# Kernel optimization log

Measured on AMD Instinct MI355X. Metric: run time of the kernel, lower is better.

## Reference

```python
import jax, jax.numpy as jnp
import numpy as np

TOP_K = 2

def setup_inputs() -> dict:
    key = jax.random.key(0)
    k1, k2 = jax.random.split(key)
    x = jax.random.normal(k1, (4, 4096, 4096), dtype=jnp.float32)
    # nn.Linear(hidden, experts, bias=False) weight: [num_experts, hidden]
    gate_w = jax.random.normal(k2, (64, 4096), dtype=jnp.float32) * (1.0 / np.sqrt(4096.0))
    return {"x": x, "gate_w": gate_w}

def reference(x, gate_w):
    # logits: [b, s, e] = x @ gate_w.T
    logits = jnp.einsum('bsh,eh->bse', x, gate_w)
    top_k_logits, top_k_indices = jax.lax.top_k(logits, TOP_K)  # [b, s, k]
    # softmax over top-k logits in float32, cast back to logits dtype
    probs = jax.nn.softmax(top_k_logits.astype(jnp.float32), axis=-1).astype(logits.dtype)
    return (logits, top_k_indices, probs)
```

## Files before the change

### kernel.cpp

```cpp
#include <hip/hip_runtime.h>
#include <math.h>

#define H 4096
#define E 64
#define BMROWS 32
#define NT 256
#define KQ 1024
#define BK 32
#define NWIN (KQ / BK)

typedef short bf16x8 __attribute__((ext_vector_type(8)));
typedef float f32x4  __attribute__((ext_vector_type(4)));

__device__ __forceinline__ unsigned f2bf_rne_u(float f) {
    unsigned u = __float_as_uint(f);
    return (u + 0x7fffu + ((u >> 16) & 1u)) >> 16;
}

__global__ __launch_bounds__(256) void convert_w(const float* __restrict__ w,
                                                 unsigned short* __restrict__ wh,
                                                 unsigned short* __restrict__ wl) {
    const int i = (blockIdx.x * 256 + threadIdx.x) * 4;
    float4 v = *(const float4*)(w + i);
    float vv[4] = {v.x, v.y, v.z, v.w};
    unsigned hh[4], ll[4];
#pragma unroll
    for (int j = 0; j < 4; ++j) {
        hh[j] = f2bf_rne_u(vv[j]);
        float r = vv[j] - __uint_as_float(hh[j] << 16);
        ll[j] = __float_as_uint(r) >> 16;
    }
    ushort4 h, l;
    h.x = (unsigned short)hh[0]; h.y = (unsigned short)hh[1];
    h.z = (unsigned short)hh[2]; h.w = (unsigned short)hh[3];
    l.x = (unsigned short)ll[0]; l.y = (unsigned short)ll[1];
    l.z = (unsigned short)ll[2]; l.w = (unsigned short)ll[3];
    *(ushort4*)(wh + i) = h;
    *(ushort4*)(wl + i) = l;
}

__device__ __forceinline__ void cvt8(const float4 a, const float4 b,
                                     bf16x8& hi, bf16x8& lo) {
    float v[8] = {a.x, a.y, a.z, a.w, b.x, b.y, b.z, b.w};
#pragma unroll
    for (int i = 0; i < 8; ++i) {
        unsigned h = f2bf_rne_u(v[i]);
        float r = v[i] - __uint_as_float(h << 16);
        unsigned l = __float_as_uint(r) >> 16;
        hi[i] = (short)h;
        lo[i] = (short)l;
    }
}

__global__ __launch_bounds__(NT, 2) void router_kernel(
    const float* __restrict__ x,
    const unsigned short* __restrict__ wh,
    const unsigned short* __restrict__ wl,
    float* __restrict__ out, int M)
{
    __shared__ __align__(16) f32x4 merge[8][4][64];

    const int t    = threadIdx.x;
    const int lane = t & 63;
    const int wk   = t >> 6;
    const int m0   = blockIdx.x * BMROWS;
    const int col  = lane & 15;
    const int quad = lane >> 4;

    const int kbase = wk * KQ + quad * 8;

    const float* xp0 = x + (size_t)(m0 + col) * H + kbase;
    const float* xp1 = x + (size_t)(m0 + 16 + col) * H + kbase;
    const unsigned short* whp = wh + (size_t)col * H + kbase;
    const unsigned short* wlp = wl + (size_t)col * H + kbase;

    f32x4 acc[2][4];
#pragma unroll
    for (int mt = 0; mt < 2; ++mt)
#pragma unroll
        for (int nt = 0; nt < 4; ++nt)
            acc[mt][nt] = (f32x4){0.0f, 0.0f, 0.0f, 0.0f};

    float4 xr[2][2];
    uint4  wrh[4], wrl[4];

    auto loadwin = [&](int win) {
        const int k = win * BK;
        xr[0][0] = *(const float4*)(xp0 + k);
        xr[0][1] = *(const float4*)(xp0 + k + 4);
        xr[1][0] = *(const float4*)(xp1 + k);
        xr[1][1] = *(const float4*)(xp1 + k + 4);
#pragma unroll
        for (int nt = 0; nt < 4; ++nt) {
            wrh[nt] = *(const uint4*)(whp + (size_t)(nt * 16) * H + k);
            wrl[nt] = *(const uint4*)(wlp + (size_t)(nt * 16) * H + k);
        }
    };

    loadwin(0);
#pragma unroll 2
    for (int win = 0; win < NWIN; ++win) {
        bf16x8 ah[2], al[2];
        cvt8(xr[0][0], xr[0][1], ah[0], al[0]);
        cvt8(xr[1][0], xr[1][1], ah[1], al[1]);
        bf16x8 bh[4], bl[4];
#pragma unroll
        for (int nt = 0; nt < 4; ++nt) {
            bh[nt] = __builtin_bit_cast(bf16x8, wrh[nt]);
            bl[nt] = __builtin_bit_cast(bf16x8, wrl[nt]);
        }

        if (win + 1 < NWIN) loadwin(win + 1);

#pragma unroll
        for (int nt = 0; nt < 4; ++nt) {
#pragma unroll
            for (int mt = 0; mt < 2; ++mt) {
                acc[mt][nt] = __builtin_amdgcn_mfma_f32_16x16x32_bf16(
                    ah[mt], bh[nt], acc[mt][nt], 0, 0, 0);
                acc[mt][nt] = __builtin_amdgcn_mfma_f32_16x16x32_bf16(
                    ah[mt], bl[nt], acc[mt][nt], 0, 0, 0);
                acc[mt][nt] = __builtin_amdgcn_mfma_f32_16x16x32_bf16(
                    al[mt], bh[nt], acc[mt][nt], 0, 0, 0);
            }
        }
    }

#pragma unroll
    for (int mt = 0; mt < 2; ++mt)
#pragma unroll
        for (int nt = 0; nt < 4; ++nt)
            merge[mt * 4 + nt][wk][lane] = acc[mt][nt];
    __syncthreads();

    if (wk != 0) return;

#pragma unroll
    for (int mt = 0; mt < 2; ++mt)
#pragma unroll
        for (int nt = 0; nt < 4; ++nt) {
#pragma unroll
            for (int w = 1; w < 4; ++w) {
                f32x4 o = merge[mt * 4 + nt][w][lane];
                acc[mt][nt] += o;
            }
        }

    float* logits   = out;
    float* idx_out  = out + (size_t)M * E;
    float* prob_out = idx_out + (size_t)M * 2;

#pragma unroll
    for (int mt = 0; mt < 2; ++mt) {
        const int mrow = m0 + mt * 16 + quad * 4;
#pragma unroll
        for (int r = 0; r < 4; ++r) {
#pragma unroll
            for (int nt = 0; nt < 4; ++nt)
                logits[(size_t)(mrow + r) * E + nt * 16 + col] = acc[mt][nt][r];

            float v1 = acc[mt][0][r], v2 = -INFINITY;
            int   i1 = col,           i2 = 0x7fffffff;
#pragma unroll
            for (int nt = 1; nt < 4; ++nt) {
                const float v = acc[mt][nt][r];
                const int   e = nt * 16 + col;
                if (v > v1)      { v2 = v1; i2 = i1; v1 = v; i1 = e; }
                else if (v > v2) { v2 = v;  i2 = e; }
            }
#pragma unroll
            for (int mask = 1; mask < 16; mask <<= 1) {
                const float ov1 = __shfl_xor(v1, mask);
                const float ov2 = __shfl_xor(v2, mask);
                const int   oi1 = __shfl_xor(i1, mask);
                const int   oi2 = __shfl_xor(i2, mask);
                const bool afirst = (v1 > ov1) || (v1 == ov1 && i1 < oi1);
                float nv1, nv2; int ni1, ni2;
                if (afirst) {
                    nv1 = v1; ni1 = i1;
                    const bool s = (v2 > ov1) || (v2 == ov1 && i2 < oi1);
                    nv2 = s ? v2 : ov1; ni2 = s ? i2 : oi1;
                } else {
                    nv1 = ov1; ni1 = oi1;
                    const bool s = (ov2 > v1) || (ov2 == v1 && oi2 < i1);
                    nv2 = s ? ov2 : v1; ni2 = s ? oi2 : i1;
                }
                v1 = nv1; v2 = nv2; i1 = ni1; i2 = ni2;
            }
            if (col == 0) {
                const int m = mrow + r;
                const float e2 = __expf(v2 - v1);
                const float d  = 1.0f + e2;
                *(float2*)(idx_out  + (size_t)m * 2) = make_float2((float)i1, (float)i2);
                *(float2*)(prob_out + (size_t)m * 2) = make_float2(1.0f / d, e2 / d);
            }
        }
    }
}

extern "C" void kernel_launch(void* const* d_in, const int* in_sizes, int n_in,
                              void* d_out, int out_size, void* d_ws, size_t ws_size,
                              hipStream_t stream) {
    const float* x = (const float*)d_in[0];
    const float* w = (const float*)d_in[1];
    unsigned short* wh = (unsigned short*)d_ws;
    unsigned short* wl = wh + (size_t)E * H;
    const int M = in_sizes[0] / H;

    hipLaunchKernelGGL(convert_w, dim3((E * H) / 1024), dim3(256), 0, stream,
                       w, wh, wl);
    hipLaunchKernelGGL(router_kernel, dim3(M / BMROWS), dim3(NT), 0, stream,
                       x, wh, wl, (float*)d_out, M);
}
```

Baseline: 407.3 us.

## Deepen x prefetch to three windows and split epilogue across two waves

The main loop now keeps x loads three windows ahead in four rotating register buffers and double-buffers the weight loads, manually unrolled by four. The goal is to hide more HBM latency on the streamed x input, which dominates traffic. The cross-wave reduction and top-2/softmax epilogue is now split so waves 0 and 1 each handle one 16-row tile instead of wave 0 doing both. The bf16 split conversion is also slightly simplified. The extra register buffers raise VGPR pressure, which may hurt occupancy under launch_bounds(256,2).

Result: no change. 403.4 us (-1.0%).

```diff
diff --git a/kernel.cpp b/kernel.cpp
--- a/kernel.cpp
+++ b/kernel.cpp
@@ -44,11 +44,11 @@
     float v[8] = {a.x, a.y, a.z, a.w, b.x, b.y, b.z, b.w};
 #pragma unroll
     for (int i = 0; i < 8; ++i) {
-        unsigned h = f2bf_rne_u(v[i]);
-        float r = v[i] - __uint_as_float(h << 16);
-        unsigned l = __float_as_uint(r) >> 16;
-        hi[i] = (short)h;
-        lo[i] = (short)l;
+        const unsigned u = __float_as_uint(v[i]);
+        const unsigned t = u + 0x7fffu + ((u >> 16) & 1u);
+        const float    r = v[i] - __uint_as_float(t & 0xffff0000u);
+        hi[i] = (short)(t >> 16);
+        lo[i] = (short)(__float_as_uint(r) >> 16);
     }
 }
 
@@ -81,49 +81,60 @@
         for (int nt = 0; nt < 4; ++nt)
             acc[mt][nt] = (f32x4){0.0f, 0.0f, 0.0f, 0.0f};
 
-    float4 xr[2][2];
-    uint4  wrh[4], wrl[4];
-
-    auto loadwin = [&](int win) {
+    float4 x0[2][2], x1[2][2], x2[2][2], x3[2][2];
+    uint4  wAh[4], wAl[4], wBh[4], wBl[4];
+
+    auto loadx_into = [&](int win, float4 (&xb)[2][2]) {
         const int k = win * BK;
-        xr[0][0] = *(const float4*)(xp0 + k);
-        xr[0][1] = *(const float4*)(xp0 + k + 4);
-        xr[1][0] = *(const float4*)(xp1 + k);
-        xr[1][1] = *(const float4*)(xp1 + k + 4);
+        xb[0][0] = *(const float4*)(xp0 + k);
+        xb[0][1] = *(const float4*)(xp0 + k + 4);
+        xb[1][0] = *(const float4*)(xp1 + k);
+        xb[1][1] = *(const float4*)(xp1 + k + 4);
+    };
+    auto loadw_into = [&](int win, uint4 (&wh_)[4], uint4 (&wl_)[4]) {
+        const int k = win * BK;
 #pragma unroll
         for (int nt = 0; nt < 4; ++nt) {
-            wrh[nt] = *(const uint4*)(whp + (size_t)(nt * 16) * H + k);
-            wrl[nt] = *(const uint4*)(wlp + (size_t)(nt * 16) * H + k);
+            wh_[nt] = *(const uint4*)(whp + (size_t)(nt * 16) * H + k);
+            wl_[nt] = *(const uint4*)(wlp + (size_t)(nt * 16) * H + k);
         }
     };
 
-    loadwin(0);
-#pragma unroll 2
-    for (int win = 0; win < NWIN; ++win) {
+    auto step = [&](int win, float4 (&xc)[2][2], float4 (&xpref)[2][2],
+                    uint4 (&whc)[4], uint4 (&wlc)[4],
+                    uint4 (&whn)[4], uint4 (&wln)[4]) {
+        if (win + 3 < NWIN) loadx_into(win + 3, xpref);
+        if (win + 1 < NWIN) loadw_into(win + 1, whn, wln);
         bf16x8 ah[2], al[2];
-        cvt8(xr[0][0], xr[0][1], ah[0], al[0]);
-        cvt8(xr[1][0], xr[1][1], ah[1], al[1]);
-        bf16x8 bh[4], bl[4];
+        cvt8(xc[0][0], xc[0][1], ah[0], al[0]);
+        cvt8(xc[1][0], xc[1][1], ah[1], al[1]);
 #pragma unroll
         for (int nt = 0; nt < 4; ++nt) {
-            bh[nt] = __builtin_bit_cast(bf16x8, wrh[nt]);
-            bl[nt] = __builtin_bit_cast(bf16x8, wrl[nt]);
-        }
-
-        if (win + 1 < NWIN) loadwin(win + 1);
-
-#pragma unroll
-        for (int nt = 0; nt < 4; ++nt) {
+            const bf16x8 bh = __builtin_bit_cast(bf16x8, whc[nt]);
+            const bf16x8 bl = __builtin_bit_cast(bf16x8, wlc[nt]);
 #pragma unroll
             for (int mt = 0; mt < 2; ++mt) {
                 acc[mt][nt] = __builtin_amdgcn_mfma_f32_16x16x32_bf16(
-                    ah[mt], bh[nt], acc[mt][nt], 0, 0, 0);
+                    ah[mt], bh, acc[mt][nt], 0, 0, 0);
                 acc[mt][nt] = __builtin_amdgcn_mfma_f32_16x16x32_bf16(
-                    ah[mt], bl[nt], acc[mt][nt], 0, 0, 0);
+                    ah[mt], bl, acc[mt][nt], 0, 0, 0);
                 acc[mt][nt] = __builtin_amdgcn_mfma_f32_16x16x32_bf16(
-                    al[mt], bh[nt], acc[mt][nt], 0, 0, 0);
+                    al[mt], bh, acc[mt][nt], 0, 0, 0);
             }
         }
+    };
+
+    loadx_into(0, x0);
+    loadx_into(1, x1);
+    loadx_into(2, x2);
+    loadw_into(0, wAh, wAl);
+
+#pragma unroll 1
+    for (int win = 0; win < NWIN; win += 4) {
+        step(win,     x0, x3, wAh, wAl, wBh, wBl);
+        step(win + 1, x1, x0, wBh, wBl, wAh, wAl);
+        step(win + 2, x2, x1, wAh, wAl, wBh, wBl);
+        step(win + 3, x3, x2, wBh, wBl, wAh, wAl);
     }
 
 #pragma unroll
@@ -133,67 +144,64 @@
             merge[mt * 4 + nt][wk][lane] = acc[mt][nt];
     __syncthreads();
 
-    if (wk != 0) return;
-
-#pragma unroll
-    for (int mt = 0; mt < 2; ++mt)
-#pragma unroll
-        for (int nt = 0; nt < 4; ++nt) {
-#pragma unroll
-            for (int w = 1; w < 4; ++w) {
-                f32x4 o = merge[mt * 4 + nt][w][lane];
-                acc[mt][nt] += o;
-            }
-        }
+    if (wk >= 2) return;
+    const int mt = wk;
+
+    f32x4 a2[4];
+#pragma unroll
+    for (int nt = 0; nt < 4; ++nt) {
+        f32x4 s = merge[mt * 4 + nt][0][lane];
+#pragma unroll
+        for (int w = 1; w < 4; ++w)
+            s += merge[mt * 4 + nt][w][lane];
+        a2[nt] = s;
+    }
 
     float* logits   = out;
     float* idx_out  = out + (size_t)M * E;
     float* prob_out = idx_out + (size_t)M * 2;
 
-#pragma unroll
-    for (int mt = 0; mt < 2; ++mt) {
-        const int mrow = m0 + mt * 16 + quad * 4;
-#pragma unroll
-        for (int r = 0; r < 4; ++r) {
-#pragma unroll
-            for (int nt = 0; nt < 4; ++nt)
-                logits[(size_t)(mrow + r) * E + nt * 16 + col] = acc[mt][nt][r];
-
-            float v1 = acc[mt][0][r], v2 = -INFINITY;
-            int   i1 = col,           i2 = 0x7fffffff;
-#pragma unroll
-            for (int nt = 1; nt < 4; ++nt) {
-                const float v = acc[mt][nt][r];
-                const int   e = nt * 16 + col;
-                if (v > v1)      { v2 = v1; i2 = i1; v1 = v; i1 = e; }
-                else if (v > v2) { v2 = v;  i2 = e; }
+    const int mrow = m0 + mt * 16 + quad * 4;
+#pragma unroll
+    for (int r = 0; r < 4; ++r) {
+#pragma unroll
+        for (int nt = 0; nt < 4; ++nt)
+            logits[(size_t)(mrow + r) * E + nt * 16 + col] = a2[nt][r];
+
+        float v1 = a2[0][r], v2 = -INFINITY;
+        int   i1 = col,      i2 = 0x7fffffff;
+#pragma unroll
+        for (int nt = 1; nt < 4; ++nt) {
+            const float v = a2[nt][r];
+            const int   e = nt * 16 + col;
+            if (v > v1)      { v2 = v1; i2 = i1; v1 = v; i1 = e; }
+            else if (v > v2) { v2 = v;  i2 = e; }
+        }
+#pragma unroll
+        for (int mask = 1; mask < 16; mask <<= 1) {
+            const float ov1 = __shfl_xor(v1, mask);
+            const float ov2 = __shfl_xor(v2, mask);
+            const int   oi1 = __shfl_xor(i1, mask);
+            const int   oi2 = __shfl_xor(i2, mask);
+            const bool afirst = (v1 > ov1) || (v1 == ov1 && i1 < oi1);
+            float nv1, nv2; int ni1, ni2;
+            if (afirst) {
+                nv1 = v1; ni1 = i1;
+                const bool s = (v2 > ov1) || (v2 == ov1 && i2 < oi1);
+                nv2 = s ? v2 : ov1; ni2 = s ? i2 : oi1;
+            } else {
+                nv1 = ov1; ni1 = oi1;
+                const bool s = (ov2 > v1) || (ov2 == v1 && oi2 < i1);
+                nv2 = s ? ov2 : v1; ni2 = s ? oi2 : i1;
             }
-#pragma unroll
-            for (int mask = 1; mask < 16; mask <<= 1) {
-                const float ov1 = __shfl_xor(v1, mask);
-                const float ov2 = __shfl_xor(v2, mask);
-                const int   oi1 = __shfl_xor(i1, mask);
-                const int   oi2 = __shfl_xor(i2, mask);
-                const bool afirst = (v1 > ov1) || (v1 == ov1 && i1 < oi1);
-                float nv1, nv2; int ni1, ni2;
-                if (afirst) {
-                    nv1 = v1; ni1 = i1;
-                    const bool s = (v2 > ov1) || (v2 == ov1 && i2 < oi1);
-                    nv2 = s ? v2 : ov1; ni2 = s ? i2 : oi1;
-                } else {
-                    nv1 = ov1; ni1 = oi1;
-                    const bool s = (ov2 > v1) || (ov2 == v1 && oi2 < i1);
-                    nv2 = s ? ov2 : v1; ni2 = s ? oi2 : i1;
-                }
-                v1 = nv1; v2 = nv2; i1 = ni1; i2 = ni2;
-            }
-            if (col == 0) {
-                const int m = mrow + r;
-                const float e2 = __expf(v2 - v1);
-                const float d  = 1.0f + e2;
-                *(float2*)(idx_out  + (size_t)m * 2) = make_float2((float)i1, (float)i2);
-                *(float2*)(prob_out + (size_t)m * 2) = make_float2(1.0f / d, e2 / d);
-            }
+            v1 = nv1; v2 = nv2; i1 = ni1; i2 = ni2;
+        }
+        if (col == 0) {
+            const int m = mrow + r;
+            const float e2 = __expf(v2 - v1);
+            const float d  = 1.0f + e2;
+            *(float2*)(idx_out  + (size_t)m * 2) = make_float2((float)i1, (float)i2);
+            *(float2*)(prob_out + (size_t)m * 2) = make_float2(1.0f / d, e2 / d);
         }
     }
 }
```
